# Kernel tuning notes

Hardware: AMD Instinct MI355X
Metric: run time of the kernel (lower is better)

Reference implementation:

```python
import jax, jax.numpy as jnp
import numpy as np

H = 16
DH = 64


def _apply_rotary(x, cos, sin):
    # x: [b, h, s, d]; cos/sin: [s, d//2] -> broadcast to [1, 1, s, d//2]
    x1 = x[..., ::2]
    x2 = x[..., 1::2]
    c = cos[None, None]
    s = sin[None, None]
    rot = jnp.stack([x1 * c - x2 * s, x1 * s + x2 * c], axis=-1)
    return rot.reshape(x.shape)


def setup_inputs() -> dict:
    key = jax.random.key(0)
    ks = jax.random.split(key, 7)
    dim = 1024
    std = 0.02
    x = jax.random.normal(ks[0], (2, 2048, dim), dtype=jnp.float32)
    persistent = jax.random.normal(ks[1], (2, 16, dim), dtype=jnp.float32)
    memory = jax.random.normal(ks[2], (2, 64, dim), dtype=jnp.float32)
    Wq = jax.random.normal(ks[3], (dim, dim), dtype=jnp.float32) * std
    Wk = jax.random.normal(ks[4], (dim, dim), dtype=jnp.float32) * std
    Wv = jax.random.normal(ks[5], (dim, dim), dtype=jnp.float32) * std
    Wo = jax.random.normal(ks[6], (dim, dim), dtype=jnp.float32) * std
    return {"x": x, "persistent": persistent, "memory": memory,
            "Wq": Wq, "Wk": Wk, "Wv": Wv, "Wo": Wo}


def reference(x, persistent, memory, Wq, Wk, Wv, Wo):
    b, L, dim = x.shape
    P = persistent.shape[1] + memory.shape[1]  # prefix_len
    full_x = jnp.concatenate([persistent, memory, x], axis=1)  # [b, P+L, dim]
    S = full_x.shape[1]
    scale = DH ** -0.5

    def proj(W):
        y = full_x @ W.T  # [b, S, dim]
        return y.reshape(b, S, H, DH).transpose(0, 2, 1, 3)  # [b, H, S, DH]

    q = proj(Wq)
    k = proj(Wk)
    v = proj(Wv)

    # RoPE only on the main (input) segment, positions starting at 0.
    pos = jnp.arange(L, dtype=jnp.float32)
    inv_freq = 1.0 / (10000.0 ** (jnp.arange(0, DH, 2, dtype=jnp.float32) / DH))
    freqs = pos[:, None] * inv_freq[None, :]  # [L, DH//2]
    cos, sin = jnp.cos(freqs), jnp.sin(freqs)

    q_main = _apply_rotary(q[:, :, P:], cos, sin)  # [b, H, L, DH]
    k = jnp.concatenate([k[:, :, :P], _apply_rotary(k[:, :, P:], cos, sin)], axis=2)

    # Only main-segment query rows affect the returned output (output[:, P:]).
    # Mask for main queries: prefix keys fully visible; causal within main.
    qi = jnp.arange(L)[:, None]
    kj = jnp.arange(S)[None, :]
    mask = (kj < P) | ((kj - P) <= qi)  # [L, S]

    scores = jnp.einsum('bhqd,bhkd->bhqk', q_main, k) * scale  # [b, H, L, S]
    scores = jnp.where(mask[None, None], scores, -jnp.inf)
    attn = jax.nn.softmax(scores, axis=-1)
    out = jnp.einsum('bhqk,bhkd->bhqd', attn, v)  # [b, H, L, DH]
    out = out.transpose(0, 2, 1, 3).reshape(b, L, dim)
    return out @ Wo.T
```

## Files before the change

### kernel.cpp

```cpp
#include <hip/hip_runtime.h>
#include <math.h>

#define BB    2
#define LL    2048
#define DIM   1024
#define NH    16
#define DHD   64
#define NPER  16
#define NMEM  64
#define PFX   80
#define SS    2128
#define MQKV  (BB*SS)
#define NQKV  3072
#define MOUT  (BB*LL)

typedef __attribute__((ext_vector_type(4)))  float f32x4;
typedef __attribute__((ext_vector_type(16))) float f32x16;
typedef __attribute__((ext_vector_type(8)))  short bf16x8;
typedef unsigned short u16;
typedef unsigned int   u32;

union I4B8 { int4 i; bf16x8 v; };

__device__ __forceinline__ u16 f2bf(float x) {
    union { float f; u32 u; } v; v.f = x;
    return (u16)((v.u + 0x7fffu + ((v.u >> 16) & 1u)) >> 16);
}
__device__ __forceinline__ u32 cvtpk(float lo, float hi) {
    u32 r; asm("v_cvt_pk_bf16_f32 %0, %1, %2" : "=v"(r) : "v"(lo), "v"(hi));
    return r;
}
__device__ __forceinline__ void gload_lds16(const void* g, void* l) {
    __builtin_amdgcn_global_load_lds(
        (__attribute__((address_space(1))) void*)(g),
        (__attribute__((address_space(3))) void*)(l), 16, 0, 0);
}

#define BARRIER()  __builtin_amdgcn_s_barrier()
#define VMCNT8()   asm volatile("s_waitcnt vmcnt(8)")

__global__ __launch_bounds__(256)
void prep_kernel(const float* __restrict__ x,  const float* __restrict__ pe,
                 const float* __restrict__ me, const float* __restrict__ Wq,
                 const float* __restrict__ Wk, const float* __restrict__ Wv,
                 const float* __restrict__ Wo,
                 u16* __restrict__ xbf, u16* __restrict__ wqkv,
                 u16* __restrict__ wobf,
                 float* __restrict__ ropeC, float* __restrict__ ropeS)
{
    const int nthr = gridDim.x * blockDim.x;
    const int t0   = blockIdx.x * blockDim.x + threadIdx.x;

    for (int g = t0; g < MQKV * (DIM / 4); g += nthr) {
        int d4  = g & 255;
        int row = g >> 8;
        int b   = row >= SS;
        int s   = row - b * SS;
        const float* src;
        if (s < NPER)     src = pe + ((size_t)(b * NPER + s)) * DIM;
        else if (s < PFX) src = me + ((size_t)(b * NMEM + (s - NPER))) * DIM;
        else              src = x  + ((size_t)(b * LL   + (s - PFX)))  * DIM;
        float4 v = *reinterpret_cast<const float4*>(src + d4 * 4);
        ushort4 o; o.x = f2bf(v.x); o.y = f2bf(v.y); o.z = f2bf(v.z); o.w = f2bf(v.w);
        *reinterpret_cast<ushort4*>(xbf + (size_t)g * 4) = o;
    }
    for (int g = t0; g < NQKV * (DIM / 4); g += nthr) {
        int row = g >> 8;
        const float* src = (row < 1024) ? (Wq + (size_t)row * DIM)
                         : (row < 2048) ? (Wk + (size_t)(row - 1024) * DIM)
                         :                (Wv + (size_t)(row - 2048) * DIM);
        float4 v = *reinterpret_cast<const float4*>(src + (g & 255) * 4);
        ushort4 o; o.x = f2bf(v.x); o.y = f2bf(v.y); o.z = f2bf(v.z); o.w = f2bf(v.w);
        *reinterpret_cast<ushort4*>(wqkv + (size_t)g * 4) = o;
    }
    for (int g = t0; g < DIM * (DIM / 4); g += nthr) {
        float4 v = *reinterpret_cast<const float4*>(Wo + (size_t)g * 4);
        ushort4 o; o.x = f2bf(v.x); o.y = f2bf(v.y); o.z = f2bf(v.z); o.w = f2bf(v.w);
        *reinterpret_cast<ushort4*>(wobf + (size_t)g * 4) = o;
    }
    for (int i = t0; i < LL * 32; i += nthr) {
        int pos = i >> 5, fi = i & 31;
        float ang = (float)pos * exp2f(-(float)fi * 0.41524101186092029f);
        ropeC[i] = cosf(ang);
        ropeS[i] = sinf(ang);
    }
}

__device__ __forceinline__ void stage_half8(const u16* __restrict__ src, int grow0,
                                            int rmax, int k0, short* ldsbase, int tid)
{
#pragma unroll
    for (int rr = 0; rr < 2; ++rr) {
        int t   = tid + rr * 512;
        int row = t >> 3;
        int c   = t & 7;
        int g = grow0 + row; if (g > rmax) g = rmax;
        gload_lds16(src + (size_t)g * DIM + k0 + ((c ^ (row & 7)) << 3),
                    ldsbase + (tid >> 6) * 512 + rr * 4096);
    }
}

__device__ __forceinline__ bf16x8 ldsfrag(const short* hb, int row, int kbyte)
{
    int byte = (row * 128 + kbyte) ^ ((row & 7) << 4);
    I4B8 t;
    t.i = *reinterpret_cast<const int4*>(reinterpret_cast<const char*>(hb) + byte);
    return t.v;
}

__global__ __launch_bounds__(512, 1)
void qkv_gemm8(const u16* __restrict__ X, const u16* __restrict__ Wq3,
               const float* __restrict__ ropeC, const float* __restrict__ ropeS,
               u16* __restrict__ qkvraw)
{
    __shared__ short Xs[2][16384] __attribute__((aligned(16)));
    __shared__ short Ws[2][16384] __attribute__((aligned(16)));

    const int tid  = threadIdx.x;
    const int lane = tid & 63;
    const int wid  = tid >> 6;
    const int wm   = wid >> 2;
    const int wn   = wid & 3;
    const int bm   = blockIdx.x * 256;
    const int bn   = blockIdx.y * 256;

    f32x4 acc[8][4];
#pragma unroll
    for (int r = 0; r < 8; ++r)
#pragma unroll
        for (int c = 0; c < 4; ++c) acc[r][c] = (f32x4)(0.f);

    stage_half8(X,   bm,       MQKV - 1, 0,  &Xs[0][0],    tid);
    stage_half8(X,   bm + 128, MQKV - 1, 0,  &Xs[0][8192], tid);
    stage_half8(Wq3, bn,       NQKV - 1, 0,  &Ws[0][0],    tid);
    stage_half8(Wq3, bn + 128, NQKV - 1, 0,  &Ws[0][8192], tid);
    stage_half8(X,   bm,       MQKV - 1, 64, &Xs[1][0],    tid);
    stage_half8(X,   bm + 128, MQKV - 1, 64, &Xs[1][8192], tid);
    stage_half8(Wq3, bn,       NQKV - 1, 64, &Ws[1][0],    tid);
    stage_half8(Wq3, bn + 128, NQKV - 1, 64, &Ws[1][8192], tid);
    VMCNT8();
    BARRIER();

    const int frow = lane & 15;
    const int fkb  = (lane >> 4) * 16;
    const int wrow = (wn & 1) * 64;
    const short* XhA[2] = { &Xs[0][0] + wm * 8192,        &Xs[1][0] + wm * 8192 };
    const short* WhA[2] = { &Ws[0][0] + (wn >> 1) * 8192, &Ws[1][0] + (wn >> 1) * 8192 };

    for (int it = 0; it < 8; ++it) {
        int ksA = it * 128 + 128; if (ksA >= 1024) ksA = 0;
        int ksB = it * 128 + 192; if (ksB >= 1024) ksB = 64;
#pragma unroll
        for (int sub = 0; sub < 2; ++sub) {
            const short* Xh = XhA[sub];
            const short* Wh = WhA[sub];
            const int kst = sub ? ksB : ksA;
            short* XsN = &Xs[sub][0];
            short* WsN = &Ws[sub][0];
            bf16x8 xfA[4][2], xfB[4][2], wfA[2][2], wfB[2][2];

#pragma unroll
            for (int r = 0; r < 4; ++r)
#pragma unroll
                for (int ks = 0; ks < 2; ++ks)
                    xfA[r][ks] = ldsfrag(Xh, r * 16 + frow, ks * 64 + fkb);
#pragma unroll
            for (int c = 0; c < 2; ++c)
#pragma unroll
                for (int ks = 0; ks < 2; ++ks)
                    wfA[c][ks] = ldsfrag(Wh, wrow + c * 16 + frow, ks * 64 + fkb);
            BARRIER();
            __builtin_amdgcn_s_setprio(1);
#pragma unroll
            for (int r = 0; r < 4; ++r)
#pragma unroll
                for (int c = 0; c < 2; ++c)
#pragma unroll
                    for (int ks = 0; ks < 2; ++ks)
                        acc[r][c] = __builtin_amdgcn_mfma_f32_16x16x32_bf16(
                            wfA[c][ks], xfA[r][ks], acc[r][c], 0, 0, 0);
            __builtin_amdgcn_s_setprio(0);
            BARRIER();

#pragma unroll
            for (int c = 0; c < 2; ++c)
#pragma unroll
                for (int ks = 0; ks < 2; ++ks)
                    wfB[c][ks] = ldsfrag(Wh, wrow + 32 + c * 16 + frow, ks * 64 + fkb);
            BARRIER();
            __builtin_amdgcn_s_setprio(1);
#pragma unroll
            for (int r = 0; r < 4; ++r)
#pragma unroll
                for (int c = 0; c < 2; ++c)
#pragma unroll
                    for (int ks = 0; ks < 2; ++ks)
                        acc[r][c + 2] = __builtin_amdgcn_mfma_f32_16x16x32_bf16(
                            wfB[c][ks], xfA[r][ks], acc[r][c + 2], 0, 0, 0);
            __builtin_amdgcn_s_setprio(0);
            BARRIER();

#pragma unroll
            for (int r = 0; r < 4; ++r)
#pragma unroll
                for (int ks = 0; ks < 2; ++ks)
                    xfB[r][ks] = ldsfrag(Xh, 64 + r * 16 + frow, ks * 64 + fkb);
            stage_half8(Wq3, bn,       NQKV - 1, kst, WsN,        tid);
            stage_half8(Wq3, bn + 128, NQKV - 1, kst, WsN + 8192, tid);
            BARRIER();
            __builtin_amdgcn_s_setprio(1);
#pragma unroll
            for (int r = 0; r < 4; ++r)
#pragma unroll
                for (int c = 0; c < 2; ++c)
#pragma unroll
                    for (int ks = 0; ks < 2; ++ks)
                        acc[r + 4][c] = __builtin_amdgcn_mfma_f32_16x16x32_bf16(
                            wfA[c][ks], xfB[r][ks], acc[r + 4][c], 0, 0, 0);
            __builtin_amdgcn_s_setprio(0);
            BARRIER();

            stage_half8(X, bm,       MQKV - 1, kst, XsN,        tid);
            stage_half8(X, bm + 128, MQKV - 1, kst, XsN + 8192, tid);
            BARRIER();
            __builtin_amdgcn_s_setprio(1);
#pragma unroll
            for (int r = 0; r < 4; ++r)
#pragma unroll
                for (int c = 0; c < 2; ++c)
#pragma unroll
                    for (int ks = 0; ks < 2; ++ks)
                        acc[r + 4][c + 2] = __builtin_amdgcn_mfma_f32_16x16x32_bf16(
                            wfB[c][ks], xfB[r][ks], acc[r + 4][c + 2], 0, 0, 0);
            __builtin_amdgcn_s_setprio(0);
            VMCNT8();
            BARRIER();
        }
    }

    const int cbase = bn + wn * 64 + ((lane >> 4) << 2);
    const int rbase = bm + wm * 128 + (lane & 15);
    const int which = bn >> 10;

#pragma unroll
    for (int xr = 0; xr < 8; ++xr) {
        const int row = rbase + xr * 16;
        if (row >= MQKV) continue;
        const int b = row >= SS;
        const int s = row - b * SS;
        const bool rope = (which != 2) && (s >= PFX);
        const int pos = s - PFX;
#pragma unroll
        for (int wc = 0; wc < 4; ++wc) {
            const int c0 = cbase + wc * 16;
            float v0 = acc[xr][wc][0], v1 = acc[xr][wc][1];
            float v2 = acc[xr][wc][2], v3 = acc[xr][wc][3];
            if (rope) {
                const int dh = c0 & 63;
                float2 cs = *reinterpret_cast<const float2*>(ropeC + pos * 32 + (dh >> 1));
                float2 sn = *reinterpret_cast<const float2*>(ropeS + pos * 32 + (dh >> 1));
                float t0 = v0 * cs.x - v1 * sn.x;
                v1 = v0 * sn.x + v1 * cs.x; v0 = t0;
                float t2 = v2 * cs.y - v3 * sn.y;
                v3 = v2 * sn.y + v3 * cs.y; v2 = t2;
            }
            ushort4 o;
            o.x = f2bf(v0); o.y = f2bf(v1); o.z = f2bf(v2); o.w = f2bf(v3);
            *reinterpret_cast<ushort4*>(&qkvraw[(size_t)row * NQKV + c0]) = o;
        }
    }
}

__global__ __launch_bounds__(256)
void wo_gemm(const u16* __restrict__ A, const u16* __restrict__ Bw,
             float* __restrict__ outp)
{
    __shared__ short As[128 * 32] __attribute__((aligned(16)));
    __shared__ short Bs[128 * 32] __attribute__((aligned(16)));

    const int tid  = threadIdx.x;
    const int lane = tid & 63;
    const int wid  = tid >> 6;
    const int wr   = wid >> 1, wc = wid & 1;
    const int bm   = blockIdx.x * 128;
    const int bn   = blockIdx.y * 128;

    f32x4 acc[4][4];
#pragma unroll
    for (int m = 0; m < 4; ++m)
#pragma unroll
        for (int n = 0; n < 4; ++n) acc[m][n] = (f32x4)(0.f);

    const int r0 = wid * 32 + (lane >> 2);
    const int cc = (lane & 3) * 8;

    for (int k0 = 0; k0 < DIM; k0 += 32) {
        gload_lds16(A + (size_t)(bm + r0) * DIM + k0 + cc, As + wid * 1024);
        gload_lds16(A + (size_t)(bm + r0 + 16) * DIM + k0 + cc, As + wid * 1024 + 512);
        gload_lds16(Bw + (size_t)(bn + r0) * DIM + k0 + cc, Bs + wid * 1024);
        gload_lds16(Bw + (size_t)(bn + r0 + 16) * DIM + k0 + cc, Bs + wid * 1024 + 512);
        __syncthreads();

        bf16x8 wf[4], xf[4];
#pragma unroll
        for (int m = 0; m < 4; ++m)
            wf[m] = *reinterpret_cast<const bf16x8*>(
                Bs + (wr * 64 + m * 16 + (lane & 15)) * 32 + (lane >> 4) * 8);
#pragma unroll
        for (int n = 0; n < 4; ++n)
            xf[n] = *reinterpret_cast<const bf16x8*>(
                As + (wc * 64 + n * 16 + (lane & 15)) * 32 + (lane >> 4) * 8);
#pragma unroll
        for (int m = 0; m < 4; ++m)
#pragma unroll
            for (int n = 0; n < 4; ++n)
                acc[m][n] = __builtin_amdgcn_mfma_f32_16x16x32_bf16(
                    wf[m], xf[n], acc[m][n], 0, 0, 0);
        __syncthreads();
    }

    const int cbase = bn + wr * 64 + ((lane >> 4) << 2);
    const int rbase = bm + wc * 64 + (lane & 15);
#pragma unroll
    for (int n = 0; n < 4; ++n) {
        const int row = rbase + n * 16;
#pragma unroll
        for (int m = 0; m < 4; ++m) {
            const int c0 = cbase + m * 16;
            *reinterpret_cast<float4*>(&outp[(size_t)row * DIM + c0]) =
                make_float4(acc[m][n][0], acc[m][n][1], acc[m][n][2], acc[m][n][3]);
        }
    }
}

__device__ __forceinline__ void attn_load_tile(
    const u16* __restrict__ kb0, const u16* __restrict__ vb0,
    int j0, int tid, int vp, int vo,
    int4& k0r, int4& k1r, int4& v0r, int4& v1r)
{
    int key0 = tid >> 3,        o0 = tid & 7;
    int c1   = tid + 256;
    int key1 = c1 >> 3,         o1 = c1 & 7;
    int jg0 = j0 + key0; if (jg0 > SS - 1) jg0 = SS - 1;
    int jg1 = j0 + key1; if (jg1 > SS - 1) jg1 = SS - 1;
    k0r = *reinterpret_cast<const int4*>(kb0 + (size_t)jg0 * NQKV + o0 * 8);
    k1r = *reinterpret_cast<const int4*>(kb0 + (size_t)jg1 * NQKV + o1 * 8);
    int ja  = j0 + 2 * vp;     if (ja  > SS - 1) ja  = SS - 1;
    int jb2 = j0 + 2 * vp + 1; if (jb2 > SS - 1) jb2 = SS - 1;
    v0r = *reinterpret_cast<const int4*>(vb0 + (size_t)ja  * NQKV + vo * 8);
    v1r = *reinterpret_cast<const int4*>(vb0 + (size_t)jb2 * NQKV + vo * 8);
}

__global__ __launch_bounds__(256, 2)
void attn_mfma(const u16* __restrict__ qkvraw, u16* __restrict__ ctx)
{
    __shared__ u16 Ks[64 * 64] __attribute__((aligned(16)));
    __shared__ u16 Vt[64 * 64] __attribute__((aligned(16)));
    __shared__ u16 Ot[4][32 * 72] __attribute__((aligned(16)));

    const int tid  = threadIdx.x;
    const int lane = tid & 63;
    const int wv   = tid >> 6;
    const int h    = lane >> 5;
    const int ql   = lane & 31;

    const int bh   = blockIdx.y;
    const int b    = bh >> 4;
    const int head = bh & 15;
    int qt = blockIdx.x;
    if (b) qt = 15 - qt;
    const int q0  = qt * 128;
    const int q0w = q0 + 32 * wv;

    const u16* qrow = qkvraw + (size_t)(b * SS + PFX + q0w + ql) * NQKV + head * DHD;
    bf16x8 qf[4];
#pragma unroll
    for (int ks = 0; ks < 4; ++ks) {
        I4B8 t; t.i = *reinterpret_cast<const int4*>(qrow + ks * 16 + h * 8);
        qf[ks] = t.v;
    }

    f32x16 oa0 = (f32x16)(0.f), oa1 = (f32x16)(0.f);
    float m = -INFINITY, l = 0.f;

    const u16* kb0 = qkvraw + (size_t)b * SS * NQKV + 1024 + head * DHD;
    const u16* vb0 = qkvraw + (size_t)b * SS * NQKV + 2048 + head * DHD;

    const int ntiles   = (PFX + q0 + 128 + 63) / 64;
    const int wave_lim = PFX + q0w + 31;
    const int vp = tid & 31;
    const int vo = tid >> 5;

    int4 rk0, rk1, rv0, rv1;
    attn_load_tile(kb0, vb0, 0, tid, vp, vo, rk0, rk1, rv0, rv1);

    for (int kt = 0; kt < ntiles; ++kt) {
        const int j0 = kt * 64;

        {
            int key0 = tid >> 3, o0 = tid & 7;
            int c1 = tid + 256;
            int key1 = c1 >> 3, o1 = c1 & 7;
            *reinterpret_cast<int4*>((char*)Ks + ((key0 * 128 + o0 * 16) ^ ((key0 & 7) << 4))) = rk0;
            *reinterpret_cast<int4*>((char*)Ks + ((key1 * 128 + o1 * 16) ^ ((key1 & 7) << 4))) = rk1;
            const u16* pa = reinterpret_cast<const u16*>(&rv0);
            const u16* pb = reinterpret_cast<const u16*>(&rv1);
#pragma unroll
            for (int d = 0; d < 8; ++d) {
                u32 wpk = (u32)pa[d] | ((u32)pb[d] << 16);
                int dh = vo * 8 + d;
                *reinterpret_cast<u32*>((char*)Vt + ((dh * 128 + vp * 4) ^ ((d & 7) << 4))) = wpk;
            }
        }
        __syncthreads();

        int4 nk0, nk1, nv0, nv1;
        attn_load_tile(kb0, vb0, j0 + 64, tid, vp, vo, nk0, nk1, nv0, nv1);

        if (j0 <= wave_lim) {
            f32x16 s0 = (f32x16)(0.f), s1 = (f32x16)(0.f);
            __builtin_amdgcn_s_setprio(1);
#pragma unroll
            for (int ks = 0; ks < 4; ++ks) {
                I4B8 k0, k1;
                k0.i = *reinterpret_cast<const int4*>(
                    (const char*)Ks + (((ql) * 128 + ks * 32 + h * 16) ^ ((ql & 7) << 4)));
                k1.i = *reinterpret_cast<const int4*>(
                    (const char*)Ks + (((32 + ql) * 128 + ks * 32 + h * 16) ^ ((ql & 7) << 4)));
                s0 = __builtin_amdgcn_mfma_f32_32x32x16_bf16(k0.v, qf[ks], s0, 0, 0, 0);
                s1 = __builtin_amdgcn_mfma_f32_32x32x16_bf16(k1.v, qf[ks], s1, 0, 0, 0);
            }
            __builtin_amdgcn_s_setprio(0);
            float sv[32];
#pragma unroll
            for (int i = 0; i < 16; ++i) { sv[i] = s0[i] * 0.125f; sv[16 + i] = s1[i] * 0.125f; }
            if (j0 + 63 > PFX + q0w) {
                const int lim = PFX + q0w + ql - j0;
#pragma unroll
                for (int i = 0; i < 32; ++i) {
                    int koff = ((i >= 16) ? 32 : 0) + (i & 3) + 8 * ((i & 15) >> 2) + 4 * h;
                    if (koff > lim) sv[i] = -INFINITY;
                }
            }
            float mt = sv[0];
#pragma unroll
            for (int i = 1; i < 32; ++i) mt = fmaxf(mt, sv[i]);
            mt = fmaxf(mt, __shfl_xor(mt, 32));
            float mn = fmaxf(m, mt);
            float f = __expf(m - mn);
            m = mn;
            float ls = 0.f;
            u32 W0[8], W1[8];
#pragma unroll
            for (int i = 0; i < 8; ++i) {
                float pa = __expf(sv[2 * i] - m);
                float pb = __expf(sv[2 * i + 1] - m);
                ls += pa + pb;
                W0[i] = cvtpk(pa, pb);
            }
#pragma unroll
            for (int i = 0; i < 8; ++i) {
                float pa = __expf(sv[16 + 2 * i] - m);
                float pb = __expf(sv[16 + 2 * i + 1] - m);
                ls += pa + pb;
                W1[i] = cvtpk(pa, pb);
            }
            ls += __shfl_xor(ls, 32);
            l = l * f + ls;
#pragma unroll
            for (int i = 0; i < 16; ++i) { oa0[i] *= f; oa1[i] *= f; }

            __builtin_amdgcn_s_setprio(1);
#pragma unroll
            for (int ks = 0; ks < 4; ++ks) {
                const int a4 = (ks & 1) * 4;
                u32 A0, A1, A2, A3;
                if (ks < 2) { A0 = W0[a4]; A1 = W0[a4 + 1]; A2 = W0[a4 + 2]; A3 = W0[a4 + 3]; }
                else        { A0 = W1[a4]; A1 = W1[a4 + 1]; A2 = W1[a4 + 2]; A3 = W1[a4 + 3]; }
                asm volatile("v_permlane32_swap_b32 %0, %1" : "+v"(A0), "+v"(A2));
                asm volatile("v_permlane32_swap_b32 %0, %1" : "+v"(A1), "+v"(A3));
                I4B8 pf; pf.i = make_int4((int)A0, (int)A1, (int)A2, (int)A3);
                I4B8 vf0, vf1;
                vf0.i = *reinterpret_cast<const int4*>(
                    (const char*)Vt + (((ql) * 128 + ks * 32 + h * 16) ^ ((ql & 7) << 4)));
                vf1.i = *reinterpret_cast<const int4*>(
                    (const char*)Vt + (((32 + ql) * 128 + ks * 32 + h * 16) ^ ((ql & 7) << 4)));
                oa0 = __builtin_amdgcn_mfma_f32_32x32x16_bf16(vf0.v, pf.v, oa0, 0, 0, 0);
                oa1 = __builtin_amdgcn_mfma_f32_32x32x16_bf16(vf1.v, pf.v, oa1, 0, 0, 0);
            }
            __builtin_amdgcn_s_setprio(0);
        }
        __syncthreads();
        rk0 = nk0; rk1 = nk1; rv0 = nv0; rv1 = nv1;
    }

    const float inv = 1.f / l;
    u16* orow = &Ot[wv][ql * 72];
#pragma unroll
    for (int i = 0; i < 8; ++i) {
        u32 w0 = cvtpk(oa0[2 * i] * inv, oa0[2 * i + 1] * inv);
        u32 w1 = cvtpk(oa1[2 * i] * inv, oa1[2 * i + 1] * inv);
        int dh0 = ((2 * i) & 3) + 8 * ((2 * i) >> 2) + 4 * h;
        *reinterpret_cast<u32*>(&orow[dh0]) = w0;
        *reinterpret_cast<u32*>(&orow[32 + dh0]) = w1;
    }
    const int rr = lane >> 1, hh = lane & 1;
    const u16* src = &Ot[wv][rr * 72 + hh * 32];
    u16* dst = ctx + ((size_t)(b * LL + q0 + 32 * wv + rr)) * DIM + head * DHD + hh * 32;
#pragma unroll
    for (int i = 0; i < 4; ++i) {
        int4 t = *reinterpret_cast<const int4*>(src + i * 8);
        *reinterpret_cast<int4*>(dst + i * 8) = t;
    }
}

extern "C" void kernel_launch(void* const* d_in, const int* in_sizes, int n_in,
                              void* d_out, int out_size, void* d_ws, size_t ws_size,
                              hipStream_t stream)
{
    const float* x  = (const float*)d_in[0];
    const float* pe = (const float*)d_in[1];
    const float* me = (const float*)d_in[2];
    const float* Wq = (const float*)d_in[3];
    const float* Wk = (const float*)d_in[4];
    const float* Wv = (const float*)d_in[5];
    const float* Wo = (const float*)d_in[6];
    float* out = (float*)d_out;

    u16* xbf  = (u16*)d_ws;
    u16* wqkv = xbf + (size_t)MQKV * DIM;
    u16* wobf = wqkv + (size_t)NQKV * DIM;
    float* ropeC = (float*)(wobf + (size_t)DIM * DIM);
    float* ropeS = ropeC + LL * 32;
    u16* qkvraw = (u16*)(ropeS + LL * 32);
    u16* ctx = qkvraw + (size_t)MQKV * NQKV;

    hipLaunchKernelGGL(prep_kernel, dim3(2048), dim3(256), 0, stream,
                       x, pe, me, Wq, Wk, Wv, Wo, xbf, wqkv, wobf, ropeC, ropeS);
    hipLaunchKernelGGL(qkv_gemm8, dim3((MQKV + 255) / 256, NQKV / 256), dim3(512), 0, stream,
                       xbf, wqkv, ropeC, ropeS, qkvraw);
    hipLaunchKernelGGL(attn_mfma, dim3(16, BB * NH), dim3(256), 0, stream,
                       qkvraw, ctx);
    hipLaunchKernelGGL(wo_gemm, dim3(MOUT / 128, DIM / 128), dim3(256), 0, stream,
                       ctx, wobf, out);
}
```

Baseline: 141.7 us.

## Halve attention query tile to 64 rows and fold softmax scale into Q

The attention kernel now uses 128-thread blocks with two waves covering 64 query rows, doubling the grid to 32 tiles per (batch, head). Each thread loads twice as much K/V per tile to make up for having fewer threads. The 1/sqrt(d) scale is moved into the QKV GEMM epilogue, so Q is pre-scaled before bf16 conversion and the per-score multiply is dropped. The aim is more blocks for better CU occupancy and finer causal load balance. The cost is that K/V tiles are reloaded more often across blocks, and rounding changes slightly because Q is scaled before the bf16 cast.

```diff
diff --git a/kernel.cpp b/kernel.cpp
--- a/kernel.cpp
+++ b/kernel.cpp
@@ -264,6 +264,9 @@
                 float t2 = v2 * cs.y - v3 * sn.y;
                 v3 = v2 * sn.y + v3 * cs.y; v2 = t2;
             }
+            if (which == 0) {
+                v0 *= 0.125f; v1 *= 0.125f; v2 *= 0.125f; v3 *= 0.125f;
+            }
             ushort4 o;
             o.x = f2bf(v0); o.y = f2bf(v1); o.z = f2bf(v2); o.w = f2bf(v3);
             *reinterpret_cast<ushort4*>(&qkvraw[(size_t)row * NQKV + c0]) = o;
@@ -335,28 +338,31 @@
 
 __device__ __forceinline__ void attn_load_tile(
     const u16* __restrict__ kb0, const u16* __restrict__ vb0,
-    int j0, int tid, int vp, int vo,
-    int4& k0r, int4& k1r, int4& v0r, int4& v1r)
-{
-    int key0 = tid >> 3,        o0 = tid & 7;
-    int c1   = tid + 256;
-    int key1 = c1 >> 3,         o1 = c1 & 7;
-    int jg0 = j0 + key0; if (jg0 > SS - 1) jg0 = SS - 1;
-    int jg1 = j0 + key1; if (jg1 > SS - 1) jg1 = SS - 1;
-    k0r = *reinterpret_cast<const int4*>(kb0 + (size_t)jg0 * NQKV + o0 * 8);
-    k1r = *reinterpret_cast<const int4*>(kb0 + (size_t)jg1 * NQKV + o1 * 8);
+    int j0, int tid, int4 kr[4], int4 vr[4])
+{
+#pragma unroll
+    for (int i = 0; i < 4; ++i) {
+        int c = tid + i * 128;
+        int key = c >> 3, o = c & 7;
+        int jg = j0 + key; if (jg > SS - 1) jg = SS - 1;
+        kr[i] = *reinterpret_cast<const int4*>(kb0 + (size_t)jg * NQKV + o * 8);
+    }
+    const int vp   = tid & 31;
+    const int voct = (tid >> 5) * 2;
     int ja  = j0 + 2 * vp;     if (ja  > SS - 1) ja  = SS - 1;
     int jb2 = j0 + 2 * vp + 1; if (jb2 > SS - 1) jb2 = SS - 1;
-    v0r = *reinterpret_cast<const int4*>(vb0 + (size_t)ja  * NQKV + vo * 8);
-    v1r = *reinterpret_cast<const int4*>(vb0 + (size_t)jb2 * NQKV + vo * 8);
-}
-
-__global__ __launch_bounds__(256, 2)
+    vr[0] = *reinterpret_cast<const int4*>(vb0 + (size_t)ja  * NQKV + voct * 8);
+    vr[1] = *reinterpret_cast<const int4*>(vb0 + (size_t)jb2 * NQKV + voct * 8);
+    vr[2] = *reinterpret_cast<const int4*>(vb0 + (size_t)ja  * NQKV + (voct + 1) * 8);
+    vr[3] = *reinterpret_cast<const int4*>(vb0 + (size_t)jb2 * NQKV + (voct + 1) * 8);
+}
+
+__global__ __launch_bounds__(128, 2)
 void attn_mfma(const u16* __restrict__ qkvraw, u16* __restrict__ ctx)
 {
     __shared__ u16 Ks[64 * 64] __attribute__((aligned(16)));
     __shared__ u16 Vt[64 * 64] __attribute__((aligned(16)));
-    __shared__ u16 Ot[4][32 * 72] __attribute__((aligned(16)));
+    __shared__ u16 Ot[2][32 * 72] __attribute__((aligned(16)));
 
     const int tid  = threadIdx.x;
     const int lane = tid & 63;
@@ -368,8 +374,8 @@
     const int b    = bh >> 4;
     const int head = bh & 15;
     int qt = blockIdx.x;
-    if (b) qt = 15 - qt;
-    const int q0  = qt * 128;
+    if (b) qt = 31 - qt;
+    const int q0  = qt * 64;
     const int q0w = q0 + 32 * wv;
 
     const u16* qrow = qkvraw + (size_t)(b * SS + PFX + q0w + ql) * NQKV + head * DHD;
@@ -386,36 +392,44 @@
     const u16* kb0 = qkvraw + (size_t)b * SS * NQKV + 1024 + head * DHD;
     const u16* vb0 = qkvraw + (size_t)b * SS * NQKV + 2048 + head * DHD;
 
-    const int ntiles   = (PFX + q0 + 128 + 63) / 64;
+    const int ntiles   = (PFX + q0 + 64 + 63) / 64;
     const int wave_lim = PFX + q0w + 31;
-    const int vp = tid & 31;
-    const int vo = tid >> 5;
-
-    int4 rk0, rk1, rv0, rv1;
-    attn_load_tile(kb0, vb0, 0, tid, vp, vo, rk0, rk1, rv0, rv1);
+    const int vp   = tid & 31;
+    const int voct = (tid >> 5) * 2;
+
+    int4 rk[4], rv[4];
+    attn_load_tile(kb0, vb0, 0, tid, rk, rv);
 
     for (int kt = 0; kt < ntiles; ++kt) {
         const int j0 = kt * 64;
 
         {
-            int key0 = tid >> 3, o0 = tid & 7;
-            int c1 = tid + 256;
-            int key1 = c1 >> 3, o1 = c1 & 7;
-            *reinterpret_cast<int4*>((char*)Ks + ((key0 * 128 + o0 * 16) ^ ((key0 & 7) << 4))) = rk0;
-            *reinterpret_cast<int4*>((char*)Ks + ((key1 * 128 + o1 * 16) ^ ((key1 & 7) << 4))) = rk1;
-            const u16* pa = reinterpret_cast<const u16*>(&rv0);
-            const u16* pb = reinterpret_cast<const u16*>(&rv1);
+            char* KD = (char*)Ks;
+#pragma unroll
+            for (int i = 0; i < 4; ++i) {
+                int c = tid + i * 128;
+                int key = c >> 3, o = c & 7;
+                *reinterpret_cast<int4*>(KD + ((key * 128 + o * 16) ^ ((key & 7) << 4))) = rk[i];
+            }
+            char* VD = (char*)Vt;
+            const u16* pa = reinterpret_cast<const u16*>(&rv[0]);
+            const u16* pb = reinterpret_cast<const u16*>(&rv[1]);
+            const u16* pc = reinterpret_cast<const u16*>(&rv[2]);
+            const u16* pd = reinterpret_cast<const u16*>(&rv[3]);
 #pragma unroll
             for (int d = 0; d < 8; ++d) {
-                u32 wpk = (u32)pa[d] | ((u32)pb[d] << 16);
-                int dh = vo * 8 + d;
-                *reinterpret_cast<u32*>((char*)Vt + ((dh * 128 + vp * 4) ^ ((d & 7) << 4))) = wpk;
+                u32 w0 = (u32)pa[d] | ((u32)pb[d] << 16);
+                u32 w1 = (u32)pc[d] | ((u32)pd[d] << 16);
+                int dh0 = voct * 8 + d;
+                int dh1 = (voct + 1) * 8 + d;
+                *reinterpret_cast<u32*>(VD + ((dh0 * 128 + vp * 4) ^ ((d & 7) << 4))) = w0;
+                *reinterpret_cast<u32*>(VD + ((dh1 * 128 + vp * 4) ^ ((d & 7) << 4))) = w1;
             }
         }
         __syncthreads();
 
-        int4 nk0, nk1, nv0, nv1;
-        attn_load_tile(kb0, vb0, j0 + 64, tid, vp, vo, nk0, nk1, nv0, nv1);
+        int4 nk[4], nv[4];
+        attn_load_tile(kb0, vb0, j0 + 64, tid, nk, nv);
 
         if (j0 <= wave_lim) {
             f32x16 s0 = (f32x16)(0.f), s1 = (f32x16)(0.f);
@@ -433,7 +447,7 @@
             __builtin_amdgcn_s_setprio(0);
             float sv[32];
 #pragma unroll
-            for (int i = 0; i < 16; ++i) { sv[i] = s0[i] * 0.125f; sv[16 + i] = s1[i] * 0.125f; }
+            for (int i = 0; i < 16; ++i) { sv[i] = s0[i]; sv[16 + i] = s1[i]; }
             if (j0 + 63 > PFX + q0w) {
                 const int lim = PFX + q0w + ql - j0;
 #pragma unroll
@@ -491,7 +505,8 @@
             __builtin_amdgcn_s_setprio(0);
         }
         __syncthreads();
-        rk0 = nk0; rk1 = nk1; rv0 = nv0; rv1 = nv1;
+#pragma unroll
+        for (int i = 0; i < 4; ++i) { rk[i] = nk[i]; rv[i] = nv[i]; }
     }
 
     const float inv = 1.f / l;
@@ -539,7 +554,7 @@
                        x, pe, me, Wq, Wk, Wv, Wo, xbf, wqkv, wobf, ropeC, ropeS);
     hipLaunchKernelGGL(qkv_gemm8, dim3((MQKV + 255) / 256, NQKV / 256), dim3(512), 0, stream,
                        xbf, wqkv, ropeC, ropeS, qkvraw);
-    hipLaunchKernelGGL(attn_mfma, dim3(16, BB * NH), dim3(256), 0, stream,
+    hipLaunchKernelGGL(attn_mfma, dim3(32, BB * NH), dim3(128), 0, stream,
                        qkvraw, ctx);
     hipLaunchKernelGGL(wo_gemm, dim3(MOUT / 128, DIM / 128), dim3(256), 0, stream,
                        ctx, wobf, out);
```

New measurement: 204.5 us. 1.44x slower.
